# Kernel tuning notes

Measured on AMD Instinct MI355X. Metric: run time of the kernel, lower is better.

Reference implementation:

```python
import jax, jax.numpy as jnp
import numpy as np

EPS = 1e-8
RESOLUTION = 32
DILATION = 1


def _stencils(resolution=RESOLUTION, dilation=DILATION):
    # interior grid of resolution^2 samples in [-1, 1]^2 (cell centers)
    lin = (np.arange(resolution) + 0.5) / resolution * 2.0 - 1.0
    gy, gx = np.meshgrid(lin, lin, indexing='ij')
    inner = np.stack([gy.ravel(), gx.ravel()], -1).astype(np.float32)
    # perimeter ring dilated outward by `dilation` cells
    scale = (resolution + 2.0 * dilation) / resolution
    mask = np.zeros((resolution, resolution), bool)
    mask[0, :] = mask[-1, :] = mask[:, 0] = mask[:, -1] = True
    outer = (inner[mask.ravel()] * scale).astype(np.float32)
    # append homogeneous coordinate (matches torch.concat with ones)
    s_in = np.concatenate([inner, np.ones((inner.shape[0], 1), np.float32)], -1)
    s_out = np.concatenate([outer, np.ones((outer.shape[0], 1), np.float32)], -1)
    return jnp.asarray(s_in), jnp.asarray(s_out)


def _bilinear(image, pos):
    # image: (H, W); pos: (..., 2) pixel coords (row, col); clamped bilinear
    H, W = image.shape
    i = pos[..., 0]
    j = pos[..., 1]
    i0 = jnp.clip(jnp.floor(i), 0, H - 2).astype(jnp.int32)
    j0 = jnp.clip(jnp.floor(j), 0, W - 2).astype(jnp.int32)
    di = jnp.clip(i - i0, 0.0, 1.0)
    dj = jnp.clip(j - j0, 0.0, 1.0)
    v00 = image[i0, j0]
    v01 = image[i0, j0 + 1]
    v10 = image[i0 + 1, j0]
    v11 = image[i0 + 1, j0 + 1]
    return (v00 * (1 - di) * (1 - dj) + v01 * (1 - di) * dj
            + v10 * di * (1 - dj) + v11 * di * dj)


def setup_inputs() -> dict:
    key = jax.random.key(0)
    k1, k2 = jax.random.split(key)
    S, P = 4, 4096
    H = W = 2048
    u = jax.random.uniform(k1, (S, P, 5), dtype=jnp.float32)
    xy = u[..., :2] * (H - 1)              # centers inside the image
    ab = 4.0 + u[..., 2:4] * 20.0          # half extents in [4, 24] px
    th = u[..., 4:5] * jnp.float32(np.pi)  # angle in [0, pi)
    points = jnp.concatenate([xy, ab, th], axis=-1)
    points_mask = jnp.ones((S, P), dtype=jnp.float32)
    position_energy_map = jax.random.normal(k2, (1, H, W), dtype=jnp.float32)
    stencil_in, stencil_out = _stencils()
    return {"points": points, "points_mask": points_mask,
            "position_energy_map": position_energy_map,
            "stencil_in": stencil_in, "stencil_out": stencil_out}


def reference(points, points_mask, position_energy_map, stencil_in, stencil_out):
    # affine_from_state: (x, y, a, b, theta) -> 2x3 affine, shape (S, P, 2, 3)
    x, y = points[..., 0], points[..., 1]
    a, b = points[..., 2], points[..., 3]
    t = points[..., 4]
    c, s = jnp.cos(t), jnp.sin(t)
    A = jnp.stack([jnp.stack([a * c, -b * s, x], -1),
                   jnp.stack([a * s, b * c, y], -1)], -2)
    # stencil coordinates in image space: (S, P, n_stencil, 2)
    coords_in = jnp.einsum('spij,nj->spni', A, stencil_in)
    coords_out = jnp.einsum('spij,nj->spni', A, stencil_out)
    img = position_energy_map[0]
    in_values = _bilinear(img, coords_in)    # (S, P, n_in)
    out_values = _bilinear(img, coords_out)  # (S, P, n_out)
    # contrast_measure: t-test-like contrast along stencil dim
    m_in, m_out = in_values.mean(-1), out_values.mean(-1)
    v_in = in_values.var(-1, ddof=1)
    v_out = out_values.var(-1, ddof=1)
    contrast = (m_in - m_out) / jnp.sqrt(v_in + v_out + EPS)
    return contrast * points_mask
```

## Files before the change

kernel.cpp:

```cpp
#include <hip/hip_runtime.h>
#include <math.h>

__global__ __launch_bounds__(256) void contrast_kernel_fast(
    const float* __restrict__ points,
    const float* __restrict__ mask,
    const float* __restrict__ img,
    float* __restrict__ out,
    int n_points)
{
    constexpr int W = 2048;
    constexpr int H = 2048;
    constexpr float fImax = (float)(H - 2);
    constexpr float fJmax = (float)(W - 2);

    const int wave = (int)((blockIdx.x * (unsigned)blockDim.x + threadIdx.x) >> 6);
    const int lane = (int)(threadIdx.x & 63u);
    if (wave >= n_points) return;

    const float* pt = points + (size_t)wave * 5;
    const float px = pt[0];
    const float py = pt[1];
    const float a  = pt[2];
    const float b  = pt[3];
    const float th = pt[4];

    float sn, cs;
    sincosf(th, &sn, &cs);
    const float A00 = a * cs, A01 = -b * sn;
    const float A10 = a * sn, A11 =  b * cs;

    const int   lr = lane >> 3;
    const int   lc = lane & 7;
    const float syb = fmaf((float)lr, 0.0625f, 0.03125f) - 1.0f;
    const float sxb = fmaf((float)lc, 0.0625f, 0.03125f) - 1.0f;

    float s0 = 0.f, q0 = 0.f, s1 = 0.f, q1 = 0.f;
    #pragma unroll
    for (int it = 0; it < 16; ++it) {
        const float dr = (float)(it >> 2) * 0.5f;
        const float dc = (float)(it & 3) * 0.5f;
        const float sy = syb + dr;
        const float sx = sxb + dc;
        const float ci = fmaf(A00, sy, fmaf(A01, sx, px));
        const float cj = fmaf(A10, sy, fmaf(A11, sx, py));
        const float fi = fminf(fmaxf(floorf(ci), 0.f), fImax);
        const float fj = fminf(fmaxf(floorf(cj), 0.f), fJmax);
        const float di = fminf(fmaxf(ci - fi, 0.f), 1.f);
        const float dj = fminf(fmaxf(cj - fj, 0.f), 1.f);
        const float* p0 = img + (((int)fi << 11) + (int)fj);
        float2 r0, r1;
        __builtin_memcpy(&r0, p0, sizeof(float2));
        __builtin_memcpy(&r1, p0 + W, sizeof(float2));
        const float top = fmaf(r0.y - r0.x, dj, r0.x);
        const float bot = fmaf(r1.y - r1.x, dj, r1.x);
        const float v   = fmaf(bot - top, di, top);
        if (it & 1) { s1 += v; q1 = fmaf(v, v, q1); }
        else        { s0 += v; q0 = fmaf(v, v, q0); }
    }
    float sum_in = s0 + s1;
    float sq_in  = q0 + q1;

    float sum_out = 0.f, sq_out = 0.f;
    #pragma unroll
    for (int base = 0; base < 124; base += 64) {
        const int n = base + lane;
        if (n < 124) {
            int row, col;
            if (n < 32)      { row = 0;                 col = n; }
            else if (n < 92) { row = 1 + ((n - 32) >> 1); col = (n & 1) * 31; }
            else             { row = 31;                col = n - 92; }
            const float sy = (fmaf((float)row, 0.0625f, 0.03125f) - 1.0f) * 1.0625f;
            const float sxo = (fmaf((float)col, 0.0625f, 0.03125f) - 1.0f) * 1.0625f;
            const float ci = fmaf(A00, sy, fmaf(A01, sxo, px));
            const float cj = fmaf(A10, sy, fmaf(A11, sxo, py));
            const float fi = fminf(fmaxf(floorf(ci), 0.f), fImax);
            const float fj = fminf(fmaxf(floorf(cj), 0.f), fJmax);
            const float di = fminf(fmaxf(ci - fi, 0.f), 1.f);
            const float dj = fminf(fmaxf(cj - fj, 0.f), 1.f);
            const float* p0 = img + (((int)fi << 11) + (int)fj);
            float2 r0, r1;
            __builtin_memcpy(&r0, p0, sizeof(float2));
            __builtin_memcpy(&r1, p0 + W, sizeof(float2));
            const float top = fmaf(r0.y - r0.x, dj, r0.x);
            const float bot = fmaf(r1.y - r1.x, dj, r1.x);
            const float v   = fmaf(bot - top, di, top);
            sum_out += v;
            sq_out = fmaf(v, v, sq_out);
        }
    }

    #pragma unroll
    for (int off = 32; off > 0; off >>= 1) {
        sum_in  += __shfl_xor(sum_in,  off);
        sq_in   += __shfl_xor(sq_in,   off);
        sum_out += __shfl_xor(sum_out, off);
        sq_out  += __shfl_xor(sq_out,  off);
    }

    if (lane == 0) {
        const float ni = 1024.f, no = 124.f;
        const float m_in  = sum_in  / ni;
        const float m_out = sum_out / no;
        const float v_in  = (sq_in  - ni * m_in  * m_in ) / (ni - 1.f);
        const float v_out = (sq_out - no * m_out * m_out) / (no - 1.f);
        const float contrast = (m_in - m_out) / sqrtf(v_in + v_out + 1e-8f);
        out[wave] = contrast * mask[wave];
    }
}

__global__ __launch_bounds__(256) void contrast_kernel_generic(
    const float* __restrict__ points, const float* __restrict__ mask,
    const float* __restrict__ img, const float* __restrict__ st_in,
    const float* __restrict__ st_out, float* __restrict__ out,
    int n_points, int n_in, int n_out, int Himg, int Wimg)
{
    const int wave = (int)((blockIdx.x * (unsigned)blockDim.x + threadIdx.x) >> 6);
    const int lane = (int)(threadIdx.x & 63u);
    if (wave >= n_points) return;
    const float* pt = points + (size_t)wave * 5;
    const float px = pt[0], py = pt[1], a = pt[2], b = pt[3], th = pt[4];
    float sn, cs; sincosf(th, &sn, &cs);
    const float A00 = a * cs, A01 = -b * sn, A10 = a * sn, A11 = b * cs;
    const float fImax = (float)(Himg - 2), fJmax = (float)(Wimg - 2);
    float sum_in = 0.f, sq_in = 0.f;
    for (int base = 0; base < n_in; base += 64) {
        const int n = base + lane;
        if (n < n_in) {
            const float sy = st_in[n * 3 + 0], sx = st_in[n * 3 + 1];
            const float ci = fmaf(A00, sy, fmaf(A01, sx, px));
            const float cj = fmaf(A10, sy, fmaf(A11, sx, py));
            const float fi = fminf(fmaxf(floorf(ci), 0.f), fImax);
            const float fj = fminf(fmaxf(floorf(cj), 0.f), fJmax);
            const float di = fminf(fmaxf(ci - fi, 0.f), 1.f);
            const float dj = fminf(fmaxf(cj - fj, 0.f), 1.f);
            const float* p0 = img + ((int)fi * Wimg + (int)fj);
            const float v00 = p0[0], v01 = p0[1], v10 = p0[Wimg], v11 = p0[Wimg + 1];
            const float top = fmaf(v01 - v00, dj, v00);
            const float bot = fmaf(v11 - v10, dj, v10);
            const float v = fmaf(bot - top, di, top);
            sum_in += v; sq_in = fmaf(v, v, sq_in);
        }
    }
    float sum_out = 0.f, sq_out = 0.f;
    for (int base = 0; base < n_out; base += 64) {
        const int n = base + lane;
        if (n < n_out) {
            const float sy = st_out[n * 3 + 0], sx = st_out[n * 3 + 1];
            const float ci = fmaf(A00, sy, fmaf(A01, sx, px));
            const float cj = fmaf(A10, sy, fmaf(A11, sx, py));
            const float fi = fminf(fmaxf(floorf(ci), 0.f), fImax);
            const float fj = fminf(fmaxf(floorf(cj), 0.f), fJmax);
            const float di = fminf(fmaxf(ci - fi, 0.f), 1.f);
            const float dj = fminf(fmaxf(cj - fj, 0.f), 1.f);
            const float* p0 = img + ((int)fi * Wimg + (int)fj);
            const float v00 = p0[0], v01 = p0[1], v10 = p0[Wimg], v11 = p0[Wimg + 1];
            const float top = fmaf(v01 - v00, dj, v00);
            const float bot = fmaf(v11 - v10, dj, v10);
            const float v = fmaf(bot - top, di, top);
            sum_out += v; sq_out = fmaf(v, v, sq_out);
        }
    }
    #pragma unroll
    for (int off = 32; off > 0; off >>= 1) {
        sum_in += __shfl_xor(sum_in, off);  sq_in += __shfl_xor(sq_in, off);
        sum_out += __shfl_xor(sum_out, off); sq_out += __shfl_xor(sq_out, off);
    }
    if (lane == 0) {
        const float ni = (float)n_in, no = (float)n_out;
        const float m_in = sum_in / ni, m_out = sum_out / no;
        const float v_in = (sq_in - ni * m_in * m_in) / (ni - 1.f);
        const float v_out = (sq_out - no * m_out * m_out) / (no - 1.f);
        const float contrast = (m_in - m_out) / sqrtf(v_in + v_out + 1e-8f);
        out[wave] = contrast * mask[wave];
    }
}

extern "C" void kernel_launch(void* const* d_in, const int* in_sizes, int n_in_bufs,
                              void* d_out, int out_size, void* d_ws, size_t ws_size,
                              hipStream_t stream) {
    (void)n_in_bufs; (void)d_ws; (void)ws_size; (void)out_size;
    const float* points = (const float*)d_in[0];
    const float* mask   = (const float*)d_in[1];
    const float* img    = (const float*)d_in[2];
    const float* st_in  = (const float*)d_in[3];
    const float* st_out = (const float*)d_in[4];
    float* out = (float*)d_out;

    const int n_points = in_sizes[0] / 5;
    const int n_in     = in_sizes[3] / 3;
    const int n_out    = in_sizes[4] / 3;
    const int hw       = in_sizes[2];

    const int waves_per_block = 4;
    const int blocks = (n_points + waves_per_block - 1) / waves_per_block;

    if (n_in == 1024 && n_out == 124 && hw == 2048 * 2048) {
        contrast_kernel_fast<<<blocks, 256, 0, stream>>>(points, mask, img, out, n_points);
    } else {
        int Wimg = 1;
        while ((long long)Wimg * Wimg < (long long)hw) Wimg <<= 1;
        const int Himg = hw / Wimg;
        contrast_kernel_generic<<<blocks, 256, 0, stream>>>(points, mask, img, st_in, st_out,
                                                            out, n_points, n_in, n_out, Himg, Wimg);
    }
}
```

Before: 116.5 us.

## Pre-gather 2x2 bilinear neighborhoods into a float4 image in workspace

Adds a pre-pass kernel that packs each pixel's 2x2 bilinear neighborhood into a float4 buffer in the workspace. The contrast kernel then does one 16-byte load per sample instead of two 8-byte loads from different rows. The cost is a full-image pass that reads 16 MB and writes about 64 MB on every call, plus a larger working set for the scattered gathers. The new path runs only when the workspace is large enough.

```diff
diff --git a/kernel.cpp b/kernel.cpp
--- a/kernel.cpp
+++ b/kernel.cpp
@@ -1,5 +1,122 @@
 #include <hip/hip_runtime.h>
 #include <math.h>
+
+
+__global__ __launch_bounds__(256) void build_img4_kernel(
+    const float* __restrict__ img,
+    float4* __restrict__ img4)
+{
+    const int t = (int)(blockIdx.x * 256u + threadIdx.x);
+    if (t >= 2047 * 2048) return;
+    const int i = t >> 11;
+    const int j = t & 2047;
+    const int jc = j > 2046 ? 2046 : j;
+    const float* p0 = img + ((i << 11) + jc);
+    float2 r0, r1;
+    __builtin_memcpy(&r0, p0, sizeof(float2));
+    __builtin_memcpy(&r1, p0 + 2048, sizeof(float2));
+    img4[t] = make_float4(r0.x, r0.y, r1.x, r1.y);
+}
+
+__global__ __launch_bounds__(256) void contrast_kernel_img4(
+    const float* __restrict__ points,
+    const float* __restrict__ mask,
+    const float4* __restrict__ img4,
+    float* __restrict__ out,
+    int n_points)
+{
+    constexpr int H = 2048, W = 2048;
+    constexpr float fImax = (float)(H - 2);
+    constexpr float fJmax = (float)(W - 2);
+
+    const int wave = (int)((blockIdx.x * (unsigned)blockDim.x + threadIdx.x) >> 6);
+    const int lane = (int)(threadIdx.x & 63u);
+    if (wave >= n_points) return;
+
+    const float* pt = points + (size_t)wave * 5;
+    const float px = pt[0];
+    const float py = pt[1];
+    const float a  = pt[2];
+    const float b  = pt[3];
+    const float th = pt[4];
+
+    float sn, cs;
+    sincosf(th, &sn, &cs);
+    const float A00 = a * cs, A01 = -b * sn;
+    const float A10 = a * sn, A11 =  b * cs;
+
+    const int   lr = lane >> 3;
+    const int   lc = lane & 7;
+    const float syb = fmaf((float)lr, 0.0625f, 0.03125f) - 1.0f;
+    const float sxb = fmaf((float)lc, 0.0625f, 0.03125f) - 1.0f;
+
+    float s0 = 0.f, q0 = 0.f, s1 = 0.f, q1 = 0.f;
+    #pragma unroll
+    for (int it = 0; it < 16; ++it) {
+        const float dr = (float)(it >> 2) * 0.5f;
+        const float dc = (float)(it & 3) * 0.5f;
+        const float sy = syb + dr;
+        const float sx = sxb + dc;
+        const float ci = fmaf(A00, sy, fmaf(A01, sx, px));
+        const float cj = fmaf(A10, sy, fmaf(A11, sx, py));
+        const float fi = fminf(fmaxf(floorf(ci), 0.f), fImax);
+        const float fj = fminf(fmaxf(floorf(cj), 0.f), fJmax);
+        const float di = fminf(fmaxf(ci - fi, 0.f), 1.f);
+        const float dj = fminf(fmaxf(cj - fj, 0.f), 1.f);
+        const float4 q = img4[((int)fi << 11) + (int)fj];
+        const float top = fmaf(q.y - q.x, dj, q.x);
+        const float bot = fmaf(q.w - q.z, dj, q.z);
+        const float v   = fmaf(bot - top, di, top);
+        if (it & 1) { s1 += v; q1 = fmaf(v, v, q1); }
+        else        { s0 += v; q0 = fmaf(v, v, q0); }
+    }
+    float sum_in = s0 + s1;
+    float sq_in  = q0 + q1;
+
+    float sum_out = 0.f, sq_out = 0.f;
+    #pragma unroll
+    for (int base = 0; base < 124; base += 64) {
+        const int n = base + lane;
+        if (n < 124) {
+            int row, col;
+            if (n < 32)      { row = 0;                   col = n; }
+            else if (n < 92) { row = 1 + ((n - 32) >> 1); col = (n & 1) * 31; }
+            else             { row = 31;                  col = n - 92; }
+            const float sy  = (fmaf((float)row, 0.0625f, 0.03125f) - 1.0f) * 1.0625f;
+            const float sxo = (fmaf((float)col, 0.0625f, 0.03125f) - 1.0f) * 1.0625f;
+            const float ci = fmaf(A00, sy, fmaf(A01, sxo, px));
+            const float cj = fmaf(A10, sy, fmaf(A11, sxo, py));
+            const float fi = fminf(fmaxf(floorf(ci), 0.f), fImax);
+            const float fj = fminf(fmaxf(floorf(cj), 0.f), fJmax);
+            const float di = fminf(fmaxf(ci - fi, 0.f), 1.f);
+            const float dj = fminf(fmaxf(cj - fj, 0.f), 1.f);
+            const float4 q = img4[((int)fi << 11) + (int)fj];
+            const float top = fmaf(q.y - q.x, dj, q.x);
+            const float bot = fmaf(q.w - q.z, dj, q.z);
+            const float v   = fmaf(bot - top, di, top);
+            sum_out += v;
+            sq_out = fmaf(v, v, sq_out);
+        }
+    }
+
+    #pragma unroll
+    for (int off = 32; off > 0; off >>= 1) {
+        sum_in  += __shfl_xor(sum_in,  off);
+        sq_in   += __shfl_xor(sq_in,   off);
+        sum_out += __shfl_xor(sum_out, off);
+        sq_out  += __shfl_xor(sq_out,  off);
+    }
+
+    if (lane == 0) {
+        const float ni = 1024.f, no = 124.f;
+        const float m_in  = sum_in  / ni;
+        const float m_out = sum_out / no;
+        const float v_in  = (sq_in  - ni * m_in  * m_in ) / (ni - 1.f);
+        const float v_out = (sq_out - no * m_out * m_out) / (no - 1.f);
+        const float contrast = (m_in - m_out) / sqrtf(v_in + v_out + 1e-8f);
+        out[wave] = contrast * mask[wave];
+    }
+}
 
 __global__ __launch_bounds__(256) void contrast_kernel_fast(
     const float* __restrict__ points,
@@ -66,10 +183,10 @@
         const int n = base + lane;
         if (n < 124) {
             int row, col;
-            if (n < 32)      { row = 0;                 col = n; }
+            if (n < 32)      { row = 0;                   col = n; }
             else if (n < 92) { row = 1 + ((n - 32) >> 1); col = (n & 1) * 31; }
-            else             { row = 31;                col = n - 92; }
-            const float sy = (fmaf((float)row, 0.0625f, 0.03125f) - 1.0f) * 1.0625f;
+            else             { row = 31;                  col = n - 92; }
+            const float sy  = (fmaf((float)row, 0.0625f, 0.03125f) - 1.0f) * 1.0625f;
             const float sxo = (fmaf((float)col, 0.0625f, 0.03125f) - 1.0f) * 1.0625f;
             const float ci = fmaf(A00, sy, fmaf(A01, sxo, px));
             const float cj = fmaf(A10, sy, fmaf(A11, sxo, py));
@@ -178,7 +295,7 @@
 extern "C" void kernel_launch(void* const* d_in, const int* in_sizes, int n_in_bufs,
                               void* d_out, int out_size, void* d_ws, size_t ws_size,
                               hipStream_t stream) {
-    (void)n_in_bufs; (void)d_ws; (void)ws_size; (void)out_size;
+    (void)n_in_bufs; (void)out_size;
     const float* points = (const float*)d_in[0];
     const float* mask   = (const float*)d_in[1];
     const float* img    = (const float*)d_in[2];
@@ -194,8 +311,17 @@
     const int waves_per_block = 4;
     const int blocks = (n_points + waves_per_block - 1) / waves_per_block;
 
+    const size_t img4_bytes = (size_t)2047 * 2048 * 16;
+
     if (n_in == 1024 && n_out == 124 && hw == 2048 * 2048) {
-        contrast_kernel_fast<<<blocks, 256, 0, stream>>>(points, mask, img, out, n_points);
+        if (d_ws != nullptr && ws_size >= img4_bytes) {
+            float4* img4 = (float4*)d_ws;
+            const int build_blocks = (2047 * 2048 + 255) / 256;
+            build_img4_kernel<<<build_blocks, 256, 0, stream>>>(img, img4);
+            contrast_kernel_img4<<<blocks, 256, 0, stream>>>(points, mask, img4, out, n_points);
+        } else {
+            contrast_kernel_fast<<<blocks, 256, 0, stream>>>(points, mask, img, out, n_points);
+        }
     } else {
         int Wimg = 1;
         while ((long long)Wimg * Wimg < (long long)hw) Wimg <<= 1;
```

After: 122.9 us. +5.5%, slower.
